# Kernel tuning notes

Hardware: AMD Instinct MI355X
Metric: run time of the kernel (lower is better)

## Reference

```python
import jax, jax.numpy as jnp
import numpy as np

N_EMBD = 2048
N_HEAD = 16
HEAD_DIM = N_EMBD // N_HEAD  # 128
ROPE_BASE = 10000.0


def _rope_cos_sin(T, dim, dtype):
    theta = 1.0 / (ROPE_BASE ** (jnp.arange(0, dim, 2, dtype=jnp.float32) / dim))  # [dim/2]
    freqs = jnp.arange(T, dtype=jnp.float32)[:, None] * theta[None, :]  # [T, dim/2]
    return jnp.cos(freqs).astype(dtype), jnp.sin(freqs).astype(dtype)


def _apply_rope(t, cos, sin):
    # t: [B,H,T,D]; interleaved (even, odd) pairs form complex numbers.
    B, H, T, D = t.shape
    tr = t.reshape(B, H, T, D // 2, 2)
    a, b = tr[..., 0], tr[..., 1]
    # (a + ib) * (cos + i sin)
    out = jnp.stack([a * cos - b * sin, a * sin + b * cos], axis=-1)
    return out.reshape(B, H, T, D)


def setup_inputs() -> dict:
    key = jax.random.key(0)
    k1, k2, k3 = jax.random.split(key, 3)
    B, T, C = 2, 2048, N_EMBD
    s = 1.0 / np.sqrt(C)
    return {
        "x": jax.random.normal(k1, (B, T, C), dtype=jnp.float32),
        "w_att": jax.random.normal(k2, (3 * C, C), dtype=jnp.float32) * s,
        "b_att": jnp.zeros((3 * C,), dtype=jnp.float32),
        "w_proj": jax.random.normal(k3, (C, C), dtype=jnp.float32) * s,
        "b_proj": jnp.zeros((C,), dtype=jnp.float32),
    }


def reference(x, w_att, b_att, w_proj, b_proj):
    B, T, C = x.shape
    H, D = N_HEAD, HEAD_DIM
    qkv = x @ w_att.T + b_att  # [B,T,3C]
    q, k, v = jnp.split(qkv, 3, axis=-1)
    # [B,T,C] -> [B,H,T,D]
    q, k, v = (t.reshape(B, T, H, D).transpose(0, 2, 1, 3) for t in (q, k, v))
    cos, sin = _rope_cos_sin(T, D, jnp.float32)  # [T, D/2]
    cos = cos[None, None]  # [1,1,T,D/2]
    sin = sin[None, None]
    q = _apply_rope(q, cos, sin)
    k = _apply_rope(k, cos, sin)
    # causal SDPA
    scale = 1.0 / np.sqrt(D)
    scores = jnp.einsum('bhqd,bhkd->bhqk', q, k) * scale
    mask = jnp.tril(jnp.ones((T, T), dtype=bool))
    scores = jnp.where(mask, scores, jnp.finfo(scores.dtype).min)
    attn = jax.nn.softmax(scores, axis=-1)
    y = jnp.einsum('bhqk,bhkd->bhqd', attn, v)  # [B,H,T,D]
    y = y.transpose(0, 2, 1, 3).reshape(B, T, C)
    return y @ w_proj.T + b_proj
```

## Files before the change

### kernel.cpp

```cpp
#include <hip/hip_runtime.h>
#include <hip/hip_bf16.h>
#include <math.h>

#define DEVI __device__ __forceinline__

typedef __attribute__((ext_vector_type(8))) short bf16x8;
typedef __attribute__((ext_vector_type(4))) float f32x4;

constexpr int Bn = 2;
constexpr int Tn = 2048;
constexpr int Cn = 2048;
constexpr int Hn = 16;
constexpr int Dn = 128;
constexpr int Mrows = Bn * Tn;
constexpr int Nqkv = 3 * Cn;
constexpr int BH = Bn * Hn;
constexpr int NKT = Cn / 32;

DEVI f32x4 mfma16x16(bf16x8 a, bf16x8 b, f32x4 c) {
    return __builtin_amdgcn_mfma_f32_16x16x32_bf16(a, b, c, 0, 0, 0);
}

DEVI bf16x8 load8(const __hip_bfloat16* p) {
    return *(const bf16x8*)p;
}

DEVI short bf16bits(float f) {
    union { __hip_bfloat16 b; short s; } u;
    u.b = __float2bfloat16(f);
    return u.s;
}

typedef const __attribute__((address_space(1))) void* gas1_t;
typedef __attribute__((address_space(3))) void* las3_t;
DEVI void stage16(const __hip_bfloat16* g, __hip_bfloat16* l) {
    __builtin_amdgcn_global_load_lds((gas1_t)g, (las3_t)l, 16, 0, 0);
}

__global__ __launch_bounds__(256) void cvt_kernel(
    const float* __restrict__ src, __hip_bfloat16* __restrict__ dst)
{
    const size_t i8 = ((size_t)blockIdx.x * 256 + threadIdx.x) * 8;
    const float4 a = *(const float4*)(src + i8);
    const float4 b = *(const float4*)(src + i8 + 4);
    union { bf16x8 v; __hip_bfloat16 h[8]; } u;
    u.h[0] = __float2bfloat16(a.x); u.h[1] = __float2bfloat16(a.y);
    u.h[2] = __float2bfloat16(a.z); u.h[3] = __float2bfloat16(a.w);
    u.h[4] = __float2bfloat16(b.x); u.h[5] = __float2bfloat16(b.y);
    u.h[6] = __float2bfloat16(b.z); u.h[7] = __float2bfloat16(b.w);
    *(bf16x8*)(dst + i8) = u.v;
}

__global__ __launch_bounds__(256) void qkv_gemm_kernel(
    const __hip_bfloat16* __restrict__ xb,
    const __hip_bfloat16* __restrict__ wab,
    const float* __restrict__ bias,
    __hip_bfloat16* __restrict__ Qo,
    __hip_bfloat16* __restrict__ Ko,
    __hip_bfloat16* __restrict__ Vt)
{
    __shared__ __align__(16) __hip_bfloat16 As[2][128 * 32];
    __shared__ __align__(16) __hip_bfloat16 Bs[2][128 * 32];
    const int tid  = threadIdx.x;
    const int lane = tid & 63;
    const int wid  = tid >> 6;
    const int quad = lane >> 4;
    const int l16  = lane & 15;
    const int bm = blockIdx.y * 128;
    const int bn = blockIdx.x * 128;
    const int wm = (wid >> 1) * 64;
    const int wn = (wid & 1) * 64;

    const int lr = lane >> 2;
    const int lc = (lane & 3) * 8;
    const int r0 = 32 * wid;
    const __hip_bfloat16* Ag0 = xb  + (size_t)(bm + r0 + lr) * Cn + lc;
    const __hip_bfloat16* Ag1 = xb  + (size_t)(bm + r0 + 16 + lr) * Cn + lc;
    const __hip_bfloat16* Bg0 = wab + (size_t)(bn + r0 + lr) * Cn + lc;
    const __hip_bfloat16* Bg1 = wab + (size_t)(bn + r0 + 16 + lr) * Cn + lc;
    const int lbase0 = r0 * 32 + lane * 8;
    const int lbase1 = (r0 + 16) * 32 + lane * 8;

    const f32x4 zero = {0.f, 0.f, 0.f, 0.f};
    f32x4 acc[4][4];
#pragma unroll
    for (int i = 0; i < 4; ++i)
#pragma unroll
        for (int j = 0; j < 4; ++j) acc[i][j] = zero;

    stage16(Ag0, &As[0][lbase0]);
    stage16(Ag1, &As[0][lbase1]);
    stage16(Bg0, &Bs[0][lbase0]);
    stage16(Bg1, &Bs[0][lbase1]);
    __syncthreads();

    for (int kt = 0; kt < NKT; ++kt) {
        const int cur = kt & 1;
        if (kt + 1 < NKT) {
            const int kn = (kt + 1) * 32;
            stage16(Ag0 + kn, &As[cur ^ 1][lbase0]);
            stage16(Ag1 + kn, &As[cur ^ 1][lbase1]);
            stage16(Bg0 + kn, &Bs[cur ^ 1][lbase0]);
            stage16(Bg1 + kn, &Bs[cur ^ 1][lbase1]);
        }
        bf16x8 af[4], bfr[4];
#pragma unroll
        for (int i = 0; i < 4; ++i)
            af[i] = load8(&As[cur][(wm + i * 16 + l16) * 32 + quad * 8]);
#pragma unroll
        for (int j = 0; j < 4; ++j)
            bfr[j] = load8(&Bs[cur][(wn + j * 16 + l16) * 32 + quad * 8]);
#pragma unroll
        for (int i = 0; i < 4; ++i)
#pragma unroll
            for (int j = 0; j < 4; ++j)
                acc[i][j] = mfma16x16(af[i], bfr[j], acc[i][j]);
        __syncthreads();
    }

#pragma unroll
    for (int j = 0; j < 4; ++j) {
        const int n = bn + wn + j * 16 + l16;
        const float bv = bias[n];
        const int sel = n >> 11;
        const int c   = n & 2047;
        const int h   = c >> 7;
        const int d   = c & 127;
#pragma unroll
        for (int i = 0; i < 4; ++i) {
#pragma unroll
            for (int r = 0; r < 4; ++r) {
                const int m = bm + wm + i * 16 + quad * 4 + r;
                const int b = m >> 11;
                const int t = m & 2047;
                const int bh = b * Hn + h;
                const __hip_bfloat16 hv = __float2bfloat16(acc[i][j][r] + bv);
                if (sel == 0)      Qo[((size_t)bh * Tn + t) * Dn + d] = hv;
                else if (sel == 1) Ko[((size_t)bh * Tn + t) * Dn + d] = hv;
                else               Vt[((size_t)bh * Dn + d) * Tn + t] = hv;
            }
        }
    }
}

__global__ __launch_bounds__(256) void rope_kernel(
    __hip_bfloat16* __restrict__ Qo,
    __hip_bfloat16* __restrict__ Ko)
{
    const size_t idx = (size_t)blockIdx.x * blockDim.x + threadIdx.x;
    const int d2 = (int)(idx & 63);
    const int t  = (int)((idx >> 6) & (size_t)(Tn - 1));
    const float inv = exp2f(-(float)d2 * (1.0f / 64.0f) * 13.287712379549449f);
    float sn, cs;
    sincosf((float)t * inv, &sn, &cs);
    const size_t base = (idx >> 6) * (size_t)Dn + (size_t)(2 * d2);
    {
        const float a = __bfloat162float(Qo[base]);
        const float b = __bfloat162float(Qo[base + 1]);
        Qo[base]     = __float2bfloat16(a * cs - b * sn);
        Qo[base + 1] = __float2bfloat16(a * sn + b * cs);
    }
    {
        const float a = __bfloat162float(Ko[base]);
        const float b = __bfloat162float(Ko[base + 1]);
        Ko[base]     = __float2bfloat16(a * cs - b * sn);
        Ko[base + 1] = __float2bfloat16(a * sn + b * cs);
    }
}

__global__ __launch_bounds__(256) void flash_kernel(
    const __hip_bfloat16* __restrict__ Qo,
    const __hip_bfloat16* __restrict__ Ko,
    const __hip_bfloat16* __restrict__ Vt,
    __hip_bfloat16* __restrict__ Y)
{
    __shared__ __align__(16) short Ks[2][32 * 136];
    __shared__ __align__(16) short Vs[2][128 * 40];
    __shared__ __align__(16) short Ps[4][16 * 40];
    const int tid  = threadIdx.x;
    const int lane = tid & 63;
    const int wid  = tid >> 6;
    const int quad = lane >> 4;
    const int l16  = lane & 15;
    const int bh   = blockIdx.x & (BH - 1);
    const int qblk = 31 - (blockIdx.x >> 5);
    const int q0w  = qblk * 64 + wid * 16;
    const int nkt  = 2 * qblk + 2;

    const __hip_bfloat16* Qb = Qo + (size_t)bh * Tn * Dn;
    const __hip_bfloat16* Kg = Ko + (size_t)bh * Tn * Dn;
    const __hip_bfloat16* Vg = Vt + (size_t)bh * Dn * Tn;
    short* P = &Ps[wid][0];

    const int krow = tid >> 3, kseg = tid & 7;
    const int vrow = tid >> 1, vseg = tid & 1;
    const __hip_bfloat16* KgT = Kg + (size_t)krow * Dn + kseg * 16;
    const __hip_bfloat16* VgT = Vg + (size_t)vrow * Tn + vseg * 16;
    short* KsT = (short*)&Ks[0][krow * 136 + kseg * 16];
    short* VsT = (short*)&Vs[0][vrow * 40 + vseg * 16];
    const int KsBuf = 32 * 136, VsBuf = 128 * 40;

    bf16x8 qf[4];
#pragma unroll
    for (int ks = 0; ks < 4; ++ks)
        qf[ks] = load8(Qb + (size_t)(q0w + l16) * Dn + ks * 32 + quad * 8);

    const f32x4 zero = {0.f, 0.f, 0.f, 0.f};
    f32x4 o[8];
#pragma unroll
    for (int j = 0; j < 8; ++j) o[j] = zero;
    float lpart[4] = {0.f, 0.f, 0.f, 0.f};
    const float scale2 = 0.12751743430267602f;

    *(bf16x8*)(KsT)     = load8((const __hip_bfloat16*)KgT);
    *(bf16x8*)(KsT + 8) = load8((const __hip_bfloat16*)KgT + 8);
    *(bf16x8*)(VsT)     = load8((const __hip_bfloat16*)VgT);
    *(bf16x8*)(VsT + 8) = load8((const __hip_bfloat16*)VgT + 8);
    __syncthreads();

    for (int kt = 0; kt < nkt; ++kt) {
        const int cur = kt & 1;
        if (kt + 1 < nkt) {
            const int kb2 = (kt + 1) * 32;
            const int nxt = (cur ^ 1);
            *(bf16x8*)(KsT + nxt * KsBuf)     = load8((const __hip_bfloat16*)KgT + (size_t)kb2 * Dn);
            *(bf16x8*)(KsT + nxt * KsBuf + 8) = load8((const __hip_bfloat16*)KgT + (size_t)kb2 * Dn + 8);
            *(bf16x8*)(VsT + nxt * VsBuf)     = load8((const __hip_bfloat16*)VgT + kb2);
            *(bf16x8*)(VsT + nxt * VsBuf + 8) = load8((const __hip_bfloat16*)VgT + kb2 + 8);
        }
        const int kb = kt * 32;
        if (kb <= q0w + 15) {
            f32x4 sc0 = zero, sc1 = zero;
#pragma unroll
            for (int ks = 0; ks < 4; ++ks) {
                bf16x8 kf0 = *(const bf16x8*)&Ks[cur][(l16) * 136 + ks * 32 + quad * 8];
                bf16x8 kf1 = *(const bf16x8*)&Ks[cur][(16 + l16) * 136 + ks * 32 + quad * 8];
                sc0 = mfma16x16(qf[ks], kf0, sc0);
                sc1 = mfma16x16(qf[ks], kf1, sc1);
            }
            if (kb + 31 <= q0w) {
#pragma unroll
                for (int r = 0; r < 4; ++r) {
                    const float p0 = exp2f(sc0[r] * scale2);
                    const float p1 = exp2f(sc1[r] * scale2);
                    lpart[r] += p0 + p1;
                    P[(quad * 4 + r) * 40 + l16]      = bf16bits(p0);
                    P[(quad * 4 + r) * 40 + 16 + l16] = bf16bits(p1);
                }
            } else {
#pragma unroll
                for (int r = 0; r < 4; ++r) {
                    const int row = q0w + quad * 4 + r;
                    const float a0 = (kb + l16      <= row) ? sc0[r] * scale2 : -INFINITY;
                    const float a1 = (kb + 16 + l16 <= row) ? sc1[r] * scale2 : -INFINITY;
                    const float p0 = exp2f(a0);
                    const float p1 = exp2f(a1);
                    lpart[r] += p0 + p1;
                    P[(quad * 4 + r) * 40 + l16]      = bf16bits(p0);
                    P[(quad * 4 + r) * 40 + 16 + l16] = bf16bits(p1);
                }
            }
            __builtin_amdgcn_sched_barrier(0);
            const bf16x8 af = *(const bf16x8*)(P + l16 * 40 + quad * 8);
#pragma unroll
            for (int j = 0; j < 8; ++j) {
                bf16x8 vf = *(const bf16x8*)&Vs[cur][(j * 16 + l16) * 40 + quad * 8];
                o[j] = mfma16x16(af, vf, o[j]);
            }
            __builtin_amdgcn_sched_barrier(0);
        }
        __syncthreads();
    }

    float invl[4];
#pragma unroll
    for (int r = 0; r < 4; ++r) {
        float s = lpart[r];
#pragma unroll
        for (int off = 1; off < 16; off <<= 1)
            s += __shfl_xor(s, off, 16);
        invl[r] = 1.0f / s;
    }

    const int b = bh >> 4;
    const int h = bh & 15;
#pragma unroll
    for (int j = 0; j < 8; ++j) {
#pragma unroll
        for (int r = 0; r < 4; ++r) {
            const int t = q0w + quad * 4 + r;
            Y[((size_t)b * Tn + t) * Cn + h * Dn + j * 16 + l16] =
                __float2bfloat16(o[j][r] * invl[r]);
        }
    }
}

__global__ __launch_bounds__(256) void proj_gemm_kernel(
    const __hip_bfloat16* __restrict__ Yb,
    const __hip_bfloat16* __restrict__ wpb,
    const float* __restrict__ bias,
    float* __restrict__ out)
{
    __shared__ __align__(16) __hip_bfloat16 As[2][128 * 32];
    __shared__ __align__(16) __hip_bfloat16 Bs[2][128 * 32];
    const int tid  = threadIdx.x;
    const int lane = tid & 63;
    const int wid  = tid >> 6;
    const int quad = lane >> 4;
    const int l16  = lane & 15;
    const int bm = blockIdx.y * 128;
    const int bn = blockIdx.x * 128;
    const int wm = (wid >> 1) * 64;
    const int wn = (wid & 1) * 64;

    const int lr = lane >> 2;
    const int lc = (lane & 3) * 8;
    const int r0 = 32 * wid;
    const __hip_bfloat16* Ag0 = Yb  + (size_t)(bm + r0 + lr) * Cn + lc;
    const __hip_bfloat16* Ag1 = Yb  + (size_t)(bm + r0 + 16 + lr) * Cn + lc;
    const __hip_bfloat16* Bg0 = wpb + (size_t)(bn + r0 + lr) * Cn + lc;
    const __hip_bfloat16* Bg1 = wpb + (size_t)(bn + r0 + 16 + lr) * Cn + lc;
    const int lbase0 = r0 * 32 + lane * 8;
    const int lbase1 = (r0 + 16) * 32 + lane * 8;

    const f32x4 zero = {0.f, 0.f, 0.f, 0.f};
    f32x4 acc[4][4];
#pragma unroll
    for (int i = 0; i < 4; ++i)
#pragma unroll
        for (int j = 0; j < 4; ++j) acc[i][j] = zero;

    stage16(Ag0, &As[0][lbase0]);
    stage16(Ag1, &As[0][lbase1]);
    stage16(Bg0, &Bs[0][lbase0]);
    stage16(Bg1, &Bs[0][lbase1]);
    __syncthreads();

    for (int kt = 0; kt < NKT; ++kt) {
        const int cur = kt & 1;
        if (kt + 1 < NKT) {
            const int kn = (kt + 1) * 32;
            stage16(Ag0 + kn, &As[cur ^ 1][lbase0]);
            stage16(Ag1 + kn, &As[cur ^ 1][lbase1]);
            stage16(Bg0 + kn, &Bs[cur ^ 1][lbase0]);
            stage16(Bg1 + kn, &Bs[cur ^ 1][lbase1]);
        }
        bf16x8 af[4], bfr[4];
#pragma unroll
        for (int i = 0; i < 4; ++i)
            af[i] = load8(&As[cur][(wm + i * 16 + l16) * 32 + quad * 8]);
#pragma unroll
        for (int j = 0; j < 4; ++j)
            bfr[j] = load8(&Bs[cur][(wn + j * 16 + l16) * 32 + quad * 8]);
#pragma unroll
        for (int i = 0; i < 4; ++i)
#pragma unroll
            for (int j = 0; j < 4; ++j)
                acc[i][j] = mfma16x16(af[i], bfr[j], acc[i][j]);
        __syncthreads();
    }

#pragma unroll
    for (int j = 0; j < 4; ++j) {
        const int n = bn + wn + j * 16 + l16;
        const float bv = bias[n];
#pragma unroll
        for (int i = 0; i < 4; ++i) {
#pragma unroll
            for (int r = 0; r < 4; ++r) {
                const int m = bm + wm + i * 16 + quad * 4 + r;
                out[(size_t)m * Cn + n] = acc[i][j][r] + bv;
            }
        }
    }
}

extern "C" void kernel_launch(void* const* d_in, const int* in_sizes, int n_in,
                              void* d_out, int out_size, void* d_ws, size_t ws_size,
                              hipStream_t stream)
{
    const float* x      = (const float*)d_in[0];
    const float* w_att  = (const float*)d_in[1];
    const float* b_att  = (const float*)d_in[2];
    const float* w_proj = (const float*)d_in[3];
    const float* b_proj = (const float*)d_in[4];
    float* out = (float*)d_out;

    const size_t per  = (size_t)BH * Tn * Dn;
    const size_t wabN = (size_t)Nqkv * Cn;
    __hip_bfloat16* Qo  = (__hip_bfloat16*)d_ws;
    __hip_bfloat16* Ko  = Qo + per;
    __hip_bfloat16* Vt  = Ko + per;
    __hip_bfloat16* xb  = Vt + per;
    __hip_bfloat16* wab = xb + per;
    __hip_bfloat16* wpb = wab + wabN;
    __hip_bfloat16* Yb  = xb;

    dim3 blk(256);
    cvt_kernel<<<dim3((Mrows * Cn) / 2048), blk, 0, stream>>>(x, xb);
    cvt_kernel<<<dim3((Nqkv * Cn) / 2048), blk, 0, stream>>>(w_att, wab);
    cvt_kernel<<<dim3((Cn * Cn) / 2048), blk, 0, stream>>>(w_proj, wpb);
    qkv_gemm_kernel<<<dim3(Nqkv / 128, Mrows / 128), blk, 0, stream>>>(
        xb, wab, b_att, Qo, Ko, Vt);
    rope_kernel<<<dim3((BH * Tn * 64) / 256), blk, 0, stream>>>(Qo, Ko);
    flash_kernel<<<dim3((Tn / 64) * BH), blk, 0, stream>>>(Qo, Ko, Vt, Yb);
    proj_gemm_kernel<<<dim3(Cn / 128, Mrows / 128), blk, 0, stream>>>(
        Yb, wpb, b_proj, out);
}
```

Measured before the change: 435.9 us.

## Restructure QKV GEMM with 256x128 tiles, triple-buffered LDS, swizzle and XCD remap

The QKV projection GEMM now runs 512-thread blocks on 256x128 output tiles, with a three-stage LDS ring fed by global_load_lds and an XOR-swizzled LDS layout. Loads are split between two MFMA phases and wrapped in barriers and s_setprio, and blocks are remapped so neighbouring tiles land on the same XCD. The aim is to hide global-load latency, cut LDS bank conflicts and improve L2 reuse. In exchange it uses more LDS per block and adds barriers, hand-tuned vmcnt waits and heavier register pressure at launch_bounds(512,4).

```diff
diff --git a/kernel.cpp b/kernel.cpp
--- a/kernel.cpp
+++ b/kernel.cpp
@@ -37,6 +37,14 @@
     __builtin_amdgcn_global_load_lds((gas1_t)g, (las3_t)l, 16, 0, 0);
 }
 
+DEVI int swzb(int o) {
+    return o ^ (((o >> 9) & 1) << 5) ^ (((o >> 7) & 1) << 4);
+}
+
+DEVI bf16x8 lds8(const short* tile, int off) {
+    return *(const bf16x8*)((const char*)tile + off);
+}
+
 __global__ __launch_bounds__(256) void cvt_kernel(
     const float* __restrict__ src, __hip_bfloat16* __restrict__ dst)
 {
@@ -51,7 +59,7 @@
     *(bf16x8*)(dst + i8) = u.v;
 }
 
-__global__ __launch_bounds__(256) void qkv_gemm_kernel(
+__global__ __launch_bounds__(512, 4) void qkv_gemm_kernel(
     const __hip_bfloat16* __restrict__ xb,
     const __hip_bfloat16* __restrict__ wab,
     const float* __restrict__ bias,
@@ -59,27 +67,37 @@
     __hip_bfloat16* __restrict__ Ko,
     __hip_bfloat16* __restrict__ Vt)
 {
-    __shared__ __align__(16) __hip_bfloat16 As[2][128 * 32];
-    __shared__ __align__(16) __hip_bfloat16 Bs[2][128 * 32];
+    __shared__ __align__(16) short As[3][256 * 32];
+    __shared__ __align__(16) short Bs[3][128 * 32];
     const int tid  = threadIdx.x;
     const int lane = tid & 63;
     const int wid  = tid >> 6;
     const int quad = lane >> 4;
     const int l16  = lane & 15;
-    const int bm = blockIdx.y * 128;
-    const int bn = blockIdx.x * 128;
-    const int wm = (wid >> 1) * 64;
-    const int wn = (wid & 1) * 64;
-
-    const int lr = lane >> 2;
-    const int lc = (lane & 3) * 8;
-    const int r0 = 32 * wid;
-    const __hip_bfloat16* Ag0 = xb  + (size_t)(bm + r0 + lr) * Cn + lc;
-    const __hip_bfloat16* Ag1 = xb  + (size_t)(bm + r0 + 16 + lr) * Cn + lc;
-    const __hip_bfloat16* Bg0 = wab + (size_t)(bn + r0 + lr) * Cn + lc;
-    const __hip_bfloat16* Bg1 = wab + (size_t)(bn + r0 + 16 + lr) * Cn + lc;
-    const int lbase0 = r0 * 32 + lane * 8;
-    const int lbase1 = (r0 + 16) * 32 + lane * 8;
+
+    const int wg = (blockIdx.x & 7) * 96 + (blockIdx.x >> 3);
+    const int bx = wg >> 4;
+    const int by = wg & 15;
+    const int bm = by * 256;
+    const int bn = bx * 128;
+
+    const int wr0 = (wid >> 1) * 64;
+    const int wc0 = (wid & 1) * 64;
+
+    const int oA0 = tid * 16;
+    const int oA1 = 8192 + tid * 16;
+    const int oB0 = tid * 16;
+    const int sA0 = swzb(oA0), sA1 = swzb(oA1), sB0 = swzb(oB0);
+    const __hip_bfloat16* Ag0 = xb  + (size_t)(bm + (sA0 >> 6)) * Cn + ((sA0 & 63) >> 1);
+    const __hip_bfloat16* Ag1 = xb  + (size_t)(bm + (sA1 >> 6)) * Cn + ((sA1 & 63) >> 1);
+    const __hip_bfloat16* Bg0 = wab + (size_t)(bn + (sB0 >> 6)) * Cn + ((sB0 & 63) >> 1);
+
+    int offA[4], offB[4];
+#pragma unroll
+    for (int f = 0; f < 4; ++f) {
+        offA[f] = swzb((wr0 + f * 16 + l16) * 64 + quad * 16);
+        offB[f] = swzb((wc0 + f * 16 + l16) * 64 + quad * 16);
+    }
 
     const f32x4 zero = {0.f, 0.f, 0.f, 0.f};
     f32x4 acc[4][4];
@@ -88,39 +106,72 @@
 #pragma unroll
         for (int j = 0; j < 4; ++j) acc[i][j] = zero;
 
-    stage16(Ag0, &As[0][lbase0]);
-    stage16(Ag1, &As[0][lbase1]);
-    stage16(Bg0, &Bs[0][lbase0]);
-    stage16(Bg1, &Bs[0][lbase1]);
-    __syncthreads();
-
+    stage16(Ag0,      (__hip_bfloat16*)&As[0][oA0 >> 1]);
+    stage16(Ag1,      (__hip_bfloat16*)&As[0][oA1 >> 1]);
+    stage16(Bg0,      (__hip_bfloat16*)&Bs[0][oB0 >> 1]);
+    stage16(Ag0 + 32, (__hip_bfloat16*)&As[1][oA0 >> 1]);
+    stage16(Ag1 + 32, (__hip_bfloat16*)&As[1][oA1 >> 1]);
+    stage16(Bg0 + 32, (__hip_bfloat16*)&Bs[1][oB0 >> 1]);
+    asm volatile("s_waitcnt vmcnt(3)" ::: "memory");
+    __builtin_amdgcn_s_barrier();
+    asm volatile("" ::: "memory");
+
+    int cur = 0, pre = 2;
     for (int kt = 0; kt < NKT; ++kt) {
-        const int cur = kt & 1;
-        if (kt + 1 < NKT) {
-            const int kn = (kt + 1) * 32;
-            stage16(Ag0 + kn, &As[cur ^ 1][lbase0]);
-            stage16(Ag1 + kn, &As[cur ^ 1][lbase1]);
-            stage16(Bg0 + kn, &Bs[cur ^ 1][lbase0]);
-            stage16(Bg1 + kn, &Bs[cur ^ 1][lbase1]);
-        }
-        bf16x8 af[4], bfr[4];
-#pragma unroll
-        for (int i = 0; i < 4; ++i)
-            af[i] = load8(&As[cur][(wm + i * 16 + l16) * 32 + quad * 8]);
-#pragma unroll
-        for (int j = 0; j < 4; ++j)
-            bfr[j] = load8(&Bs[cur][(wn + j * 16 + l16) * 32 + quad * 8]);
-#pragma unroll
-        for (int i = 0; i < 4; ++i)
-#pragma unroll
-            for (int j = 0; j < 4; ++j)
-                acc[i][j] = mfma16x16(af[i], bfr[j], acc[i][j]);
-        __syncthreads();
+        const short* At = &As[cur][0];
+        const short* Bt = &Bs[cur][0];
+        const int kg = (kt + 2) * 32;
+        if (kt + 2 < NKT) {
+            stage16(Ag0 + kg, (__hip_bfloat16*)&As[pre][oA0 >> 1]);
+            stage16(Ag1 + kg, (__hip_bfloat16*)&As[pre][oA1 >> 1]);
+        }
+        bf16x8 a0 = lds8(At, offA[0]);
+        bf16x8 a1 = lds8(At, offA[1]);
+        bf16x8 a2 = lds8(At, offA[2]);
+        bf16x8 a3 = lds8(At, offA[3]);
+        bf16x8 b0 = lds8(Bt, offB[0]);
+        bf16x8 b1 = lds8(Bt, offB[1]);
+        __builtin_amdgcn_s_barrier();
+        __builtin_amdgcn_s_setprio(1);
+        acc[0][0] = mfma16x16(a0, b0, acc[0][0]);
+        acc[1][0] = mfma16x16(a1, b0, acc[1][0]);
+        acc[2][0] = mfma16x16(a2, b0, acc[2][0]);
+        acc[3][0] = mfma16x16(a3, b0, acc[3][0]);
+        acc[0][1] = mfma16x16(a0, b1, acc[0][1]);
+        acc[1][1] = mfma16x16(a1, b1, acc[1][1]);
+        acc[2][1] = mfma16x16(a2, b1, acc[2][1]);
+        acc[3][1] = mfma16x16(a3, b1, acc[3][1]);
+        __builtin_amdgcn_s_setprio(0);
+        __builtin_amdgcn_s_barrier();
+        if (kt + 2 < NKT)
+            stage16(Bg0 + kg, (__hip_bfloat16*)&Bs[pre][oB0 >> 1]);
+        bf16x8 b2 = lds8(Bt, offB[2]);
+        bf16x8 b3 = lds8(Bt, offB[3]);
+        __builtin_amdgcn_s_barrier();
+        __builtin_amdgcn_s_setprio(1);
+        acc[0][2] = mfma16x16(a0, b2, acc[0][2]);
+        acc[1][2] = mfma16x16(a1, b2, acc[1][2]);
+        acc[2][2] = mfma16x16(a2, b2, acc[2][2]);
+        acc[3][2] = mfma16x16(a3, b2, acc[3][2]);
+        acc[0][3] = mfma16x16(a0, b3, acc[0][3]);
+        acc[1][3] = mfma16x16(a1, b3, acc[1][3]);
+        acc[2][3] = mfma16x16(a2, b3, acc[2][3]);
+        acc[3][3] = mfma16x16(a3, b3, acc[3][3]);
+        __builtin_amdgcn_s_setprio(0);
+        if (kt < NKT - 2) {
+            asm volatile("s_waitcnt vmcnt(3)" ::: "memory");
+        } else {
+            asm volatile("s_waitcnt vmcnt(0)" ::: "memory");
+        }
+        __builtin_amdgcn_s_barrier();
+        asm volatile("" ::: "memory");
+        cur = (cur == 2) ? 0 : cur + 1;
+        pre = (pre == 2) ? 0 : pre + 1;
     }
 
 #pragma unroll
     for (int j = 0; j < 4; ++j) {
-        const int n = bn + wn + j * 16 + l16;
+        const int n = bn + wc0 + j * 16 + l16;
         const float bv = bias[n];
         const int sel = n >> 11;
         const int c   = n & 2047;
@@ -130,7 +181,7 @@
         for (int i = 0; i < 4; ++i) {
 #pragma unroll
             for (int r = 0; r < 4; ++r) {
-                const int m = bm + wm + i * 16 + quad * 4 + r;
+                const int m = bm + wr0 + i * 16 + quad * 4 + r;
                 const int b = m >> 11;
                 const int t = m & 2047;
                 const int bh = b * Hn + h;
@@ -400,7 +451,7 @@
     cvt_kernel<<<dim3((Mrows * Cn) / 2048), blk, 0, stream>>>(x, xb);
     cvt_kernel<<<dim3((Nqkv * Cn) / 2048), blk, 0, stream>>>(w_att, wab);
     cvt_kernel<<<dim3((Cn * Cn) / 2048), blk, 0, stream>>>(w_proj, wpb);
-    qkv_gemm_kernel<<<dim3(Nqkv / 128, Mrows / 128), blk, 0, stream>>>(
+    qkv_gemm_kernel<<<dim3((Mrows / 256) * (Nqkv / 128)), dim3(512), 0, stream>>>(
         xb, wab, b_att, Qo, Ko, Vt);
     rope_kernel<<<dim3((BH * Tn * 64) / 256), blk, 0, stream>>>(Qo, Ko);
     flash_kernel<<<dim3((Tn / 64) * BH), blk, 0, stream>>>(Qo, Ko, Vt, Yb);
```

After: 469.2 us. +7.6%, slower.

## Stage flash-attention K/V tiles with direct global-to-LDS loads and XOR swizzle

Applied to the files above, without the earlier changes.

The flash kernel previously loaded K and V tiles into registers and then wrote them to padded shared-memory arrays. It now uses global_load_lds to copy 16-byte chunks straight into LDS, in unpadded tiles with an XOR swizzle on the chunk index to avoid bank conflicts. The MFMA operand reads use precomputed swizzled byte offsets to match. This removes the VGPR round trip and the LDS store instructions, and lets the next tile's loads overlap compute asynchronously. It depends on the compiler inserting the right vmcnt waits before the barrier, and on the swizzle read pattern actually being conflict-free.

```diff
diff --git a/kernel.cpp b/kernel.cpp
--- a/kernel.cpp
+++ b/kernel.cpp
@@ -35,6 +35,10 @@
 typedef __attribute__((address_space(3))) void* las3_t;
 DEVI void stage16(const __hip_bfloat16* g, __hip_bfloat16* l) {
     __builtin_amdgcn_global_load_lds((gas1_t)g, (las3_t)l, 16, 0, 0);
+}
+
+DEVI bf16x8 lds8(const short* tile, int byte_off) {
+    return *(const bf16x8*)((const char*)tile + byte_off);
 }
 
 __global__ __launch_bounds__(256) void cvt_kernel(
@@ -174,8 +178,8 @@
     const __hip_bfloat16* __restrict__ Vt,
     __hip_bfloat16* __restrict__ Y)
 {
-    __shared__ __align__(16) short Ks[2][32 * 136];
-    __shared__ __align__(16) short Vs[2][128 * 40];
+    __shared__ __align__(16) short Ks[2][32 * 128];
+    __shared__ __align__(16) short Vs[2][128 * 32];
     __shared__ __align__(16) short Ps[4][16 * 40];
     const int tid  = threadIdx.x;
     const int lane = tid & 63;
@@ -192,13 +196,18 @@
     const __hip_bfloat16* Vg = Vt + (size_t)bh * Dn * Tn;
     short* P = &Ps[wid][0];
 
-    const int krow = tid >> 3, kseg = tid & 7;
-    const int vrow = tid >> 1, vseg = tid & 1;
-    const __hip_bfloat16* KgT = Kg + (size_t)krow * Dn + kseg * 16;
-    const __hip_bfloat16* VgT = Vg + (size_t)vrow * Tn + vseg * 16;
-    short* KsT = (short*)&Ks[0][krow * 136 + kseg * 16];
-    short* VsT = (short*)&Vs[0][vrow * 40 + vseg * 16];
-    const int KsBuf = 32 * 136, VsBuf = 128 * 40;
+    const int kr = tid >> 4;
+    const int ksl = (tid & 15) ^ kr;
+    const __hip_bfloat16* KgA = Kg + (size_t)kr * Dn + ksl * 8;
+    const int vr = tid >> 2;
+    const int vsl = (tid & 3) ^ ((vr >> 1) & 3);
+    const __hip_bfloat16* VgA = Vg + (size_t)vr * Tn + vsl * 8;
+
+    int koff[4];
+#pragma unroll
+    for (int ks = 0; ks < 4; ++ks)
+        koff[ks] = l16 * 256 + ((((ks * 4 + quad) ^ l16) & 15) << 4);
+    const int vkey = ((quad ^ ((l16 >> 1) & 3)) << 4);
 
     bf16x8 qf[4];
 #pragma unroll
@@ -212,29 +221,29 @@
     float lpart[4] = {0.f, 0.f, 0.f, 0.f};
     const float scale2 = 0.12751743430267602f;
 
-    *(bf16x8*)(KsT)     = load8((const __hip_bfloat16*)KgT);
-    *(bf16x8*)(KsT + 8) = load8((const __hip_bfloat16*)KgT + 8);
-    *(bf16x8*)(VsT)     = load8((const __hip_bfloat16*)VgT);
-    *(bf16x8*)(VsT + 8) = load8((const __hip_bfloat16*)VgT + 8);
+    stage16(KgA,            (__hip_bfloat16*)&Ks[0][tid * 8]);
+    stage16(KgA + 16 * Dn,  (__hip_bfloat16*)&Ks[0][2048 + tid * 8]);
+    stage16(VgA,            (__hip_bfloat16*)&Vs[0][tid * 8]);
+    stage16(VgA + 64 * Tn,  (__hip_bfloat16*)&Vs[0][2048 + tid * 8]);
     __syncthreads();
 
     for (int kt = 0; kt < nkt; ++kt) {
         const int cur = kt & 1;
         if (kt + 1 < nkt) {
             const int kb2 = (kt + 1) * 32;
-            const int nxt = (cur ^ 1);
-            *(bf16x8*)(KsT + nxt * KsBuf)     = load8((const __hip_bfloat16*)KgT + (size_t)kb2 * Dn);
-            *(bf16x8*)(KsT + nxt * KsBuf + 8) = load8((const __hip_bfloat16*)KgT + (size_t)kb2 * Dn + 8);
-            *(bf16x8*)(VsT + nxt * VsBuf)     = load8((const __hip_bfloat16*)VgT + kb2);
-            *(bf16x8*)(VsT + nxt * VsBuf + 8) = load8((const __hip_bfloat16*)VgT + kb2 + 8);
+            const int nxt = cur ^ 1;
+            stage16(KgA + (size_t)kb2 * Dn,           (__hip_bfloat16*)&Ks[nxt][tid * 8]);
+            stage16(KgA + (size_t)(kb2 + 16) * Dn,    (__hip_bfloat16*)&Ks[nxt][2048 + tid * 8]);
+            stage16(VgA + kb2,                        (__hip_bfloat16*)&Vs[nxt][tid * 8]);
+            stage16(VgA + 64 * Tn + kb2,              (__hip_bfloat16*)&Vs[nxt][2048 + tid * 8]);
         }
         const int kb = kt * 32;
         if (kb <= q0w + 15) {
             f32x4 sc0 = zero, sc1 = zero;
 #pragma unroll
             for (int ks = 0; ks < 4; ++ks) {
-                bf16x8 kf0 = *(const bf16x8*)&Ks[cur][(l16) * 136 + ks * 32 + quad * 8];
-                bf16x8 kf1 = *(const bf16x8*)&Ks[cur][(16 + l16) * 136 + ks * 32 + quad * 8];
+                bf16x8 kf0 = lds8(&Ks[cur][0], koff[ks]);
+                bf16x8 kf1 = lds8(&Ks[cur][0], koff[ks] + 4096);
                 sc0 = mfma16x16(qf[ks], kf0, sc0);
                 sc1 = mfma16x16(qf[ks], kf1, sc1);
             }
@@ -264,7 +273,7 @@
             const bf16x8 af = *(const bf16x8*)(P + l16 * 40 + quad * 8);
 #pragma unroll
             for (int j = 0; j < 8; ++j) {
-                bf16x8 vf = *(const bf16x8*)&Vs[cur][(j * 16 + l16) * 40 + quad * 8];
+                bf16x8 vf = lds8(&Vs[cur][0], (j * 16 + l16) * 64 + vkey);
                 o[j] = mfma16x16(af, vf, o[j]);
             }
             __builtin_amdgcn_sched_barrier(0);
```

Result: no change. 432.9 us (-0.7%).
